# Optimization experiments

Measured on AMD Instinct MI355X. Metric: run time of the kernel, lower is better.

Reference implementation:

```python
import jax, jax.numpy as jnp
import numpy as np

SIM = 100      # topk k
GCH = SIM + 1  # group size after concat
LCH = 80       # low-rank mid channels
D = 96         # embed dim


def setup_inputs() -> dict:
    key = jax.random.key(0)
    ks = jax.random.split(key, 14)
    b, N, W, p = 1, 4, 16, 128
    def lin(kw, kb, out_f, in_f):
        s = 1.0 / np.sqrt(in_f)
        w = jax.random.uniform(kw, (out_f, in_f), minval=-s, maxval=s, dtype=jnp.float32)
        bb = jax.random.uniform(kb, (out_f,), minval=-s, maxval=s, dtype=jnp.float32)
        return w, bb
    attn = jax.random.normal(ks[0], (b, N, W, 1, p, p), dtype=jnp.float32)
    v = jax.random.normal(ks[1], (b, N, W, 1, p, D), dtype=jnp.float32)
    mb = jax.random.normal(ks[2], (LCH, 1), dtype=jnp.float32)
    w_sub, b_sub = lin(ks[3], ks[4], LCH, GCH)
    w_up, b_up = lin(ks[5], ks[6], GCH, LCH)
    w_q, b_q = lin(ks[7], ks[8], D, D)
    w_k, b_k = lin(ks[9], ks[10], D, D)
    w_o, b_o = lin(ks[11], ks[12], D, D)
    return {"attn": attn, "v": v, "mb": mb, "w_sub": w_sub, "b_sub": b_sub,
            "w_up": w_up, "b_up": b_up, "w_q": w_q, "b_q": b_q,
            "w_k": w_k, "b_k": b_k, "w_o": w_o, "b_o": b_o}


def reference(attn, v, mb, w_sub, b_sub, w_up, b_up, w_q, b_q, w_k, b_k, w_o, b_o):
    b, N, W, _, p, _ = attn.shape
    c = v.shape[-1]
    # topk + scatter(binary mask) + boolean-compact gather == gather v rows at
    # ascending-sorted topk indices (boolean masking preserves index order).
    _, idx = jax.lax.top_k(attn, SIM)            # [b,N,W,1,p,SIM]
    idx = jnp.sort(idx[:, :, :, 0], axis=-1)     # [b,N,W,p,SIM]
    vq = v[:, :, :, 0]                            # [b,N,W,p,c]
    bI = jnp.arange(b)[:, None, None, None, None]
    nI = jnp.arange(N)[None, :, None, None, None]
    wI = jnp.arange(W)[None, None, :, None, None]
    gathered = vq[bI, nI, wI, idx]                # [b,N,W,p,SIM,c]
    group3d = jnp.concatenate([vq[:, :, :, :, None, :], gathered], axis=4)  # [b,N,W,p,GCH,c]
    # ChannelAttention (memory_blocks=1): pool over c, low-rank memory bank
    y = jnp.mean(group3d, axis=-1)                # [b,N,W,p,GCH]
    lr = y @ w_sub.T + b_sub                      # [b,N,W,p,LCH]
    f1 = (lr @ mb) * (LCH ** -0.5)                # [b,N,W,p,1]
    f_dic = jax.nn.softmax(f1[..., None, :], axis=-1)   # [b,N,W,p,1,1] == 1
    y1 = f_dic * mb[:, 0]                         # [b,N,W,p,1,LCH]
    scale = jax.nn.sigmoid(y1 @ w_up.T + b_up)    # [b,N,W,p,1,GCH]
    scale = scale.reshape(b, N, W, p, GCH, 1)     # matches torch .view(b,N,Nwin,p,n,-1)
    g = group3d * scale
    # StructuralSelfAttention (num_heads=1): query = group element 0, keys/values = rest
    x = g[:, :, :, :, :1, :]                      # [b,N,W,p,1,c]
    yk = g[:, :, :, :, 1:, :]                     # [b,N,W,p,SIM,c]
    q = x @ w_q.T + b_q
    k = yk @ w_k.T + b_k
    scores = jnp.einsum('bnwpqc,bnwpkc->bnwpqk', q, k) / jnp.sqrt(jnp.float32(c))
    wgt = jax.nn.softmax(scores, axis=-1)
    out = jnp.einsum('bnwpqk,bnwpkc->bnwpqc', wgt, yk)  # v = y (no v_proj in source)
    out = out.reshape(b, N, W, p, c)
    return out @ w_o.T + b_o
```

## Files before the change

kernel.cpp:

```cpp
#include <hip/hip_runtime.h>
#include <hip/hip_bf16.h>

#define NW 64
#define P 128
#define D 96
#define PD (P*D)
#define GCH 101
#define SIM 100
#define LCH 80
#define RSQRT96 0.10206207261596577f

#define WS_SCALE 0
#define WS_Q     128
#define WS_KT    (128 + 786432)
#define WS_VO    (128 + 2*786432)

typedef unsigned long long ull;

__device__ __forceinline__ ull make_key(float a, int idx) {
  unsigned u = __float_as_uint(a);
  unsigned msk = (u & 0x80000000u) ? 0xFFFFFFFFu : 0x80000000u;
  return (((ull)(u ^ msk)) << 32) | (unsigned)(127 - idx);
}

__global__ __launch_bounds__(128, 2) void proj_kernel(const float* __restrict__ v,
    const float* __restrict__ wq, const float* __restrict__ bq,
    const float* __restrict__ wk, const float* __restrict__ wo,
    const float* __restrict__ mb, const float* __restrict__ w_up,
    const float* __restrict__ b_up, float* __restrict__ ws) {
  int bid = blockIdx.x;
  int xcd = bid & 7;
  int m = bid >> 3;
  int g = m / 12;
  int rem = m - g * 12;
  int nw = (g << 3) | xcd;
  int pj = rem >> 2, rh = rem & 3;
  const float* W = (pj == 0) ? wq : (pj == 1) ? wk : wo;
  __shared__ float sWt[96 * 100];
  __shared__ float sV[32 * 97];
  int t = threadIdx.x;
  int ty = t >> 3;
  int tx = t & 7;

  for (int k = 0; k < 72; ++k) {
    int idx = t + 128 * k;
    int c = idx / 96, d = idx - c * 96;
    sWt[d * 100 + c] = W[idx];
  }
  const float* Vg = v + (size_t)nw * PD + rh * (32 * D);
#pragma unroll
  for (int i = 0; i < 6; ++i) {
    int idx = (t + 128 * i) * 4;
    float4 x = *(const float4*)(Vg + idx);
    int r = idx / 96, d = idx - r * 96;
    float* p = &sV[r * 97 + d];
    p[0] = x.x; p[1] = x.y; p[2] = x.z; p[3] = x.w;
  }
  float scale0 = 0.f;
  if (pj == 0) {
    float a = b_up[0];
    for (int j = 0; j < LCH; ++j) a += w_up[j] * mb[j];
    scale0 = 1.f / (1.f + __expf(-a));
  }
  __syncthreads();

  float acc[2][12];
#pragma unroll
  for (int a = 0; a < 2; ++a)
#pragma unroll
    for (int j = 0; j < 12; ++j) acc[a][j] = 0.f;

  for (int d = 0; d < 96; ++d) {
    float va0 = sV[(ty * 2 + 0) * 97 + d];
    float va1 = sV[(ty * 2 + 1) * 97 + d];
    const float4* wp = (const float4*)&sWt[d * 100 + tx * 12];
    float4 w0 = wp[0], w1 = wp[1], w2 = wp[2];
    float wb[12] = {w0.x,w0.y,w0.z,w0.w, w1.x,w1.y,w1.z,w1.w, w2.x,w2.y,w2.z,w2.w};
#pragma unroll
    for (int j = 0; j < 12; ++j) {
      acc[0][j] += va0 * wb[j];
      acc[1][j] += va1 * wb[j];
    }
  }

  if (pj == 1) {
    float* ktp = ws + WS_KT + nw * PD;
#pragma unroll
    for (int a = 0; a < 2; ++a) {
      int r = rh * 32 + ty * 2 + a;
#pragma unroll
      for (int j = 0; j < 12; ++j)
        ktp[(tx * 12 + j) * P + r] = acc[a][j];
    }
  } else {
    float* outp = ws + ((pj == 0) ? WS_Q : WS_VO) + nw * PD + (rh * 32) * D;
    float4 bq4[3];
    if (pj == 0) {
      const float4* bp = (const float4*)(bq + tx * 12);
      bq4[0] = bp[0]; bq4[1] = bp[1]; bq4[2] = bp[2];
    }
#pragma unroll
    for (int a = 0; a < 2; ++a) {
      float* orow = outp + (ty * 2 + a) * D + tx * 12;
#pragma unroll
      for (int q = 0; q < 3; ++q) {
        float4 o;
        o.x = acc[a][4*q+0]; o.y = acc[a][4*q+1];
        o.z = acc[a][4*q+2]; o.w = acc[a][4*q+3];
        if (pj == 0) {
          o.x = scale0 * o.x + bq4[q].x; o.y = scale0 * o.y + bq4[q].y;
          o.z = scale0 * o.z + bq4[q].z; o.w = scale0 * o.w + bq4[q].w;
        }
        *(float4*)(orow + 4 * q) = o;
      }
    }
  }

  if (bid == 0 && t < GCH) {
    float a = b_up[t];
    for (int j = 0; j < LCH; ++j) a += w_up[t * LCH + j] * mb[j];
    ws[WS_SCALE + t] = 1.f / (1.f + __expf(-a));
  }
}

__global__ __launch_bounds__(64, 2) void attn_kernel(const float* __restrict__ attn,
    const float* __restrict__ bo, const float* __restrict__ ws,
    float* __restrict__ out) {
  int bid = blockIdx.x;
  int lane = threadIdx.x;
  int xcd = bid & 7;
  int nw = ((bid >> 9) << 3) | xcd;
  int rt = (bid >> 3) & 63;
  int p0 = rt * 2;
  const float* Kt  = ws + WS_KT + nw * PD;
  const float* VO  = ws + WS_VO + nw * PD;
  const float* Qb  = ws + WS_Q  + nw * PD + p0 * D;
  const float* Ab  = attn + (size_t)(nw * P + p0) * P;
  const float* scl = ws + WS_SCALE;

  ull ke[2], ko[2];
#pragma unroll
  for (int r = 0; r < 2; ++r) {
    float2 a2 = ((const float2*)(Ab + r * P))[lane];
    ke[r] = make_key(a2.x, 2 * lane);
    ko[r] = make_key(a2.y, 2 * lane + 1);
  }

  int ce[2] = {0, 0}, co_[2] = {0, 0};
  for (int jb = 0; jb < P; jb += 8) {
    float aj[2][8];
#pragma unroll
    for (int r = 0; r < 2; ++r)
#pragma unroll
      for (int i = 0; i < 8; ++i) aj[r][i] = Ab[r * P + jb + i];
#pragma unroll
    for (int i = 0; i < 8; ++i) {
      int j = jb + i;
#pragma unroll
      for (int r = 0; r < 2; ++r) {
        ull kj = make_key(aj[r][i], j);
        ce[r]  += (kj > ke[r]) ? 1 : 0;
        co_[r] += (kj > ko[r]) ? 1 : 0;
      }
    }
  }

  float se[2] = {0, 0}, so[2] = {0, 0};
  for (int cb = 0; cb < D; cb += 8) {
    float q[2][8];
#pragma unroll
    for (int r = 0; r < 2; ++r)
#pragma unroll
      for (int i = 0; i < 8; ++i) q[r][i] = Qb[r * D + cb + i];
#pragma unroll
    for (int i = 0; i < 8; ++i) {
      float2 kv = ((const float2*)(Kt + (cb + i) * P))[lane];
#pragma unroll
      for (int r = 0; r < 2; ++r) {
        se[r] += q[r][i] * kv.x;
        so[r] += q[r][i] * kv.y;
      }
    }
  }

  float te[2], to[2];
  ull lm = (1ull << lane) - 1ull;
#pragma unroll
  for (int r = 0; r < 2; ++r) {
    bool kpe = ce[r] < SIM, kpo = co_[r] < SIM;
    ull be = __ballot(kpe), bo_ = __ballot(kpo);
    int pe = __popcll(be & lm) + __popcll(bo_ & lm);
    int po = pe + (kpe ? 1 : 0);
    float sve = kpe ? scl[1 + pe] : 0.f;
    float svo = kpo ? scl[1 + po] : 0.f;
    float xe = kpe ? sve * se[r] * RSQRT96 : -1e30f;
    float xo = kpo ? svo * so[r] * RSQRT96 : -1e30f;
    float mx = fmaxf(xe, xo);
#pragma unroll
    for (int off = 1; off < 64; off <<= 1) mx = fmaxf(mx, __shfl_xor(mx, off));
    float ee = kpe ? __expf(xe - mx) : 0.f;
    float eo = kpo ? __expf(xo - mx) : 0.f;
    float s = ee + eo;
#pragma unroll
    for (int off = 1; off < 64; off <<= 1) s += __shfl_xor(s, off);
    float inv = 1.f / s;
    te[r] = ee * inv * sve;
    to[r] = eo * inv * svo;
  }

  int lc = (lane < 48) ? lane : 47;
  float2 o0 = {0.f, 0.f}, o1 = {0.f, 0.f};
#pragma unroll 8
  for (int j = 0; j < P; ++j) {
    float2 vo = ((const float2*)(VO + j * D))[lc];
    int h = j >> 1;
    float tv0 = __int_as_float(__builtin_amdgcn_readlane(
        __float_as_int((j & 1) ? to[0] : te[0]), h));
    float tv1 = __int_as_float(__builtin_amdgcn_readlane(
        __float_as_int((j & 1) ? to[1] : te[1]), h));
    o0.x += tv0 * vo.x; o0.y += tv0 * vo.y;
    o1.x += tv1 * vo.x; o1.y += tv1 * vo.y;
  }
  if (lane < 48) {
    float2 bb = ((const float2*)bo)[lane];
    float* op = out + (size_t)(nw * P + p0) * D;
    float2 r0; r0.x = o0.x + bb.x; r0.y = o0.y + bb.y;
    float2 r1; r1.x = o1.x + bb.x; r1.y = o1.y + bb.y;
    ((float2*)(op + 0 * D))[lane] = r0;
    ((float2*)(op + 1 * D))[lane] = r1;
  }
}

extern "C" void kernel_launch(void* const* d_in, const int* in_sizes, int n_in,
                              void* d_out, int out_size, void* d_ws, size_t ws_size,
                              hipStream_t stream) {
  const float* attn = (const float*)d_in[0];
  const float* v    = (const float*)d_in[1];
  const float* mb   = (const float*)d_in[2];
  const float* w_up = (const float*)d_in[5];
  const float* b_up = (const float*)d_in[6];
  const float* w_q  = (const float*)d_in[7];
  const float* b_q  = (const float*)d_in[8];
  const float* w_k  = (const float*)d_in[9];
  const float* w_o  = (const float*)d_in[11];
  const float* b_o  = (const float*)d_in[12];
  float* out = (float*)d_out;
  float* ws = (float*)d_ws;

  hipLaunchKernelGGL(proj_kernel, dim3(768), dim3(128), 0, stream,
                     v, w_q, b_q, w_k, w_o, mb, w_up, b_up, ws);
  hipLaunchKernelGGL(attn_kernel, dim3(4096), dim3(64), 0, stream,
                     attn, b_o, ws, out);
}
```

Baseline: 64.76 us.

## Pack four wavefronts per attn block, stage softmax weights in LDS

```diff
diff --git a/kernel.cpp b/kernel.cpp
--- a/kernel.cpp
+++ b/kernel.cpp
@@ -60,7 +60,7 @@
   if (pj == 0) {
     float a = b_up[0];
     for (int j = 0; j < LCH; ++j) a += w_up[j] * mb[j];
-    scale0 = 1.f / (1.f + __expf(-a));
+    scale0 = RSQRT96 / (1.f + __expf(-a));
   }
   __syncthreads();
 
@@ -98,6 +98,11 @@
     if (pj == 0) {
       const float4* bp = (const float4*)(bq + tx * 12);
       bq4[0] = bp[0]; bq4[1] = bp[1]; bq4[2] = bp[2];
+#pragma unroll
+      for (int q = 0; q < 3; ++q) {
+        bq4[q].x *= RSQRT96; bq4[q].y *= RSQRT96;
+        bq4[q].z *= RSQRT96; bq4[q].w *= RSQRT96;
+      }
     }
 #pragma unroll
     for (int a = 0; a < 2; ++a) {
@@ -123,15 +128,19 @@
   }
 }
 
-__global__ __launch_bounds__(64, 2) void attn_kernel(const float* __restrict__ attn,
+__global__ __launch_bounds__(256) void attn_kernel(const float* __restrict__ attn,
     const float* __restrict__ bo, const float* __restrict__ ws,
     float* __restrict__ out) {
   int bid = blockIdx.x;
-  int lane = threadIdx.x;
   int xcd = bid & 7;
-  int nw = ((bid >> 9) << 3) | xcd;
-  int rt = (bid >> 3) & 63;
-  int p0 = rt * 2;
+  int k = (bid >> 3) & 15;
+  int g = bid >> 7;
+  int nw = (g << 3) | xcd;
+  int wv = threadIdx.x >> 6;
+  int lane = threadIdx.x & 63;
+  int p0 = (k * 4 + wv) * 2;
+  __shared__ float sT[4][2][128];
+
   const float* Kt  = ws + WS_KT + nw * PD;
   const float* VO  = ws + WS_VO + nw * PD;
   const float* Qb  = ws + WS_Q  + nw * PD + p0 * D;
@@ -183,7 +192,6 @@
     }
   }
 
-  float te[2], to[2];
   ull lm = (1ull << lane) - 1ull;
 #pragma unroll
   for (int r = 0; r < 2; ++r) {
@@ -193,8 +201,8 @@
     int po = pe + (kpe ? 1 : 0);
     float sve = kpe ? scl[1 + pe] : 0.f;
     float svo = kpo ? scl[1 + po] : 0.f;
-    float xe = kpe ? sve * se[r] * RSQRT96 : -1e30f;
-    float xo = kpo ? svo * so[r] * RSQRT96 : -1e30f;
+    float xe = kpe ? sve * se[r] : -1e30f;
+    float xo = kpo ? svo * so[r] : -1e30f;
     float mx = fmaxf(xe, xo);
 #pragma unroll
     for (int off = 1; off < 64; off <<= 1) mx = fmaxf(mx, __shfl_xor(mx, off));
@@ -204,22 +212,24 @@
 #pragma unroll
     for (int off = 1; off < 64; off <<= 1) s += __shfl_xor(s, off);
     float inv = 1.f / s;
-    te[r] = ee * inv * sve;
-    to[r] = eo * inv * svo;
+    float2 tw; tw.x = ee * inv * sve; tw.y = eo * inv * svo;
+    ((float2*)sT[wv][r])[lane] = tw;
   }
 
   int lc = (lane < 48) ? lane : 47;
   float2 o0 = {0.f, 0.f}, o1 = {0.f, 0.f};
-#pragma unroll 8
-  for (int j = 0; j < P; ++j) {
-    float2 vo = ((const float2*)(VO + j * D))[lc];
-    int h = j >> 1;
-    float tv0 = __int_as_float(__builtin_amdgcn_readlane(
-        __float_as_int((j & 1) ? to[0] : te[0]), h));
-    float tv1 = __int_as_float(__builtin_amdgcn_readlane(
-        __float_as_int((j & 1) ? to[1] : te[1]), h));
-    o0.x += tv0 * vo.x; o0.y += tv0 * vo.y;
-    o1.x += tv1 * vo.x; o1.y += tv1 * vo.y;
+#pragma unroll 2
+  for (int jb = 0; jb < P; jb += 4) {
+    float4 t0 = *(const float4*)&sT[wv][0][jb];
+    float4 t1 = *(const float4*)&sT[wv][1][jb];
+    float tb0[4] = {t0.x, t0.y, t0.z, t0.w};
+    float tb1[4] = {t1.x, t1.y, t1.z, t1.w};
+#pragma unroll
+    for (int jj = 0; jj < 4; ++jj) {
+      float2 vo = ((const float2*)(VO + (jb + jj) * D))[lc];
+      o0.x += tb0[jj] * vo.x; o0.y += tb0[jj] * vo.y;
+      o1.x += tb1[jj] * vo.x; o1.y += tb1[jj] * vo.y;
+    }
   }
   if (lane < 48) {
     float2 bb = ((const float2*)bo)[lane];
@@ -249,6 +259,6 @@
 
   hipLaunchKernelGGL(proj_kernel, dim3(768), dim3(128), 0, stream,
                      v, w_q, b_q, w_k, w_o, mb, w_up, b_up, ws);
-  hipLaunchKernelGGL(attn_kernel, dim3(4096), dim3(64), 0, stream,
+  hipLaunchKernelGGL(attn_kernel, dim3(1024), dim3(256), 0, stream,
                      attn, b_o, ws, out);
 }
```

Result: slower. 81.10 us (+25.2%).
